# Kernel optimization log

Hardware: AMD Instinct MI355X
Metric: run time of the kernel (lower is better)

## Reference

```python
import math
import jax, jax.numpy as jnp
import numpy as np

S, K, Q, N, D, H = 512, 512, 64, 262144, 256, 8
DH = D // H
EPS = 1e-5


def layer_norm(x, g, b):
    mu = jnp.mean(x, axis=-1, keepdims=True)
    var = jnp.mean((x - mu) ** 2, axis=-1, keepdims=True)
    return (x - mu) / jnp.sqrt(var + EPS) * g + b


def setup_inputs() -> dict:
    key = jax.random.key(0)
    ks = jax.random.split(key, 12)
    s = 1.0 / math.sqrt(D)
    x = jax.random.normal(ks[0], (N, D), dtype=jnp.float32)
    target_ids = jax.random.randint(ks[1], (S, K), 0, N)
    # unique query slots per sample (matches torch per-slot overwrite with distinct ids)
    perm = jax.vmap(lambda k: jax.random.permutation(k, K))(jax.random.split(ks[2], S))
    add_ids = perm[:, :Q]
    return {
        "x": x,
        "target_ids": target_ids,
        "add_ids": add_ids,
        "Wq": jax.random.uniform(ks[3], (D, D), jnp.float32, -s, s),
        "bq": jnp.zeros((D,), jnp.float32),
        "Wk": jax.random.uniform(ks[4], (D, D), jnp.float32, -s, s),
        "bk": jnp.zeros((D,), jnp.float32),
        "Wv": jax.random.uniform(ks[5], (D, D), jnp.float32, -s, s),
        "bv": jnp.zeros((D,), jnp.float32),
        "g1": jnp.ones((D,), jnp.float32),
        "b1": jnp.zeros((D,), jnp.float32),
        "Wl": jax.random.uniform(ks[6], (D, D), jnp.float32, -s, s),
        "bl": jnp.zeros((D,), jnp.float32),
        "g2": jnp.ones((D,), jnp.float32),
        "b2": jnp.zeros((D,), jnp.float32),
    }


def reference(x, target_ids, add_ids, Wq, bq, Wk, bk, Wv, bv, g1, b1, Wl, bl, g2, b2):
    # gather per-sample node subsets
    key_t = x[target_ids]                                   # [S, K, D]
    query = jnp.take_along_axis(key_t, add_ids[:, :, None], axis=1)  # [S, Q, D]
    # MAB projections
    Qp = (query @ Wq.T + bq).reshape(S, Q, H, DH)
    Kp = (key_t @ Wk.T + bk).reshape(S, K, H, DH)
    Vp = (key_t @ Wv.T + bv).reshape(S, K, H, DH)
    # attention with original scaling by sqrt(dim_V) (full D, not per-head)
    scores = jnp.einsum("sqhd,skhd->shqk", Qp, Kp) / math.sqrt(D)
    A = jax.nn.softmax(scores, axis=-1)
    out = Qp + jnp.einsum("shqk,skhd->sqhd", A, Vp)          # residual on Q_
    out = out.reshape(S, Q, D)
    out = layer_norm(out, g1, b1)
    out = out + jax.nn.relu(out @ Wl.T + bl)
    out = layer_norm(out, g2, b2)                            # [S, Q, D]
    # scatter back into per-sample slots, then residual with key
    x_fuse = jnp.zeros((S, K, D), out.dtype)
    x_fuse = x_fuse.at[jnp.arange(S)[:, None], add_ids].set(out)
    x_fuse = x_fuse + key_t
    return x_fuse.reshape(S * K, D)
```

## Files before the change

### kernel.cpp

```cpp
#include <hip/hip_runtime.h>

#define S_ 512
#define K_ 512
#define Q_ 64
#define D_ 256
#define H_ 8
#define SK_ (S_*K_)
#define SQ_ (S_*Q_)

typedef float f32x4 __attribute__((ext_vector_type(4)));
typedef short bf16x8 __attribute__((ext_vector_type(8)));
typedef short bf16x4 __attribute__((ext_vector_type(4)));

__device__ __forceinline__ short f2bf(float f) {
  unsigned u = __builtin_bit_cast(unsigned, f);
  u += 0x7fffu + ((u >> 16) & 1u);
  return (short)(u >> 16);
}
__device__ __forceinline__ float bf2f(short s) {
  unsigned u = ((unsigned)(unsigned short)s) << 16;
  return __builtin_bit_cast(float, u);
}

__device__ __forceinline__ void async_copy16(short* lds, const short* g) {
  __builtin_amdgcn_global_load_lds(
      (const __attribute__((address_space(1))) void*)g,
      (__attribute__((address_space(3))) void*)lds, 16, 0, 0);
}

__global__ void cvt_w_kernel(const float* Wq, const float* Wk, const float* Wv,
                             const float* Wl, short* out) {
  int i = blockIdx.x * 256 + threadIdx.x;
  const float* src = (i < 65536) ? Wq : (i < 131072) ? Wk : (i < 196608) ? Wv : Wl;
  out[i] = f2bf(src[i & 65535]);
}

__global__ void expand_kernel(const short* kb, float* dout) {
  int g = blockIdx.x * 256 + threadIdx.x;
  bf16x8 v = *(const bf16x8*)(kb + (size_t)g * 8);
  f32x4 a, b;
#pragma unroll
  for (int j = 0; j < 4; j++) { a[j] = bf2f(v[j]); b[j] = bf2f(v[j + 4]); }
  *(f32x4*)(dout + (size_t)g * 8) = a;
  *(f32x4*)(dout + (size_t)g * 8 + 4) = b;
}

__global__ __launch_bounds__(256, 2) void gkv_kernel(const float* x, const int* tid,
                                                     const short* Wkb, const float* bkb,
                                                     const short* Wvb, const float* bvb,
                                                     short* kb, short* Kt, short* Vt) {
  __shared__ short As[128 * 256];
  int t = threadIdx.x;
  int w = t >> 6, lane = t & 63, quad = lane >> 4, l16 = lane & 15;
  int rbase0 = blockIdx.x * 128;
  int colbase = w * 64;

#pragma unroll
  for (int i = 0; i < 16; i++) {
    int g = i * 256 + t;
    int row = g >> 5, c = g & 31;
    int m = rbase0 + row;
    int src = tid[m];
    const float* xp = x + (size_t)src * 256 + c * 8;
    f32x4 v0 = *(const f32x4*)xp;
    f32x4 v1 = *(const f32x4*)(xp + 4);
    bf16x8 o;
#pragma unroll
    for (int j = 0; j < 4; j++) { o[j] = f2bf(v0[j]); o[j + 4] = f2bf(v1[j]); }
    *(bf16x8*)(kb + (size_t)m * 256 + c * 8) = o;
    *(bf16x8*)(As + row * 256 + (c ^ (row & 15)) * 8) = o;
  }
  __syncthreads();

#pragma unroll 1
  for (int p = 0; p < 2; p++) {
    const short* Wb = p ? Wvb : Wkb;
    const float* bias = p ? bvb : bkb;
    bf16x8 b[4][8];
#pragma unroll
    for (int nt = 0; nt < 4; nt++)
#pragma unroll
      for (int kk = 0; kk < 8; kk++)
        b[nt][kk] = *(const bf16x8*)(Wb + (colbase + nt * 16 + l16) * 256 + kk * 32 + quad * 8);
    float bv4[4];
#pragma unroll
    for (int nt = 0; nt < 4; nt++) bv4[nt] = bias[colbase + nt * 16 + l16];

    for (int mt = 0; mt < 8; mt++) {
      bf16x8 a[8];
#pragma unroll
      for (int kk = 0; kk < 8; kk++)
        a[kk] = *(const bf16x8*)(As + (mt * 16 + l16) * 256 + (((kk * 4 + quad) ^ l16) * 8));
      f32x4 acc[4];
#pragma unroll
      for (int nt = 0; nt < 4; nt++) acc[nt] = (f32x4){bv4[nt], bv4[nt], bv4[nt], bv4[nt]};
#pragma unroll
      for (int kk = 0; kk < 8; kk++)
#pragma unroll
        for (int nt = 0; nt < 4; nt++)
          acc[nt] = __builtin_amdgcn_mfma_f32_16x16x32_bf16(a[kk], b[nt][kk], acc[nt], 0, 0, 0);

      int rbase = rbase0 + mt * 16;
      int s = rbase >> 9;
      int keyb = (rbase & 511) + quad * 4;
      if (p == 0) {
#pragma unroll
        for (int nt = 0; nt < 4; nt++) {
          int col = colbase + nt * 16 + l16;
          int h = col >> 5, dh = col & 31;
          size_t basek = ((size_t)(s * 8 + h) * 512 + keyb) * 32 + dh;
#pragma unroll
          for (int r = 0; r < 4; r++) Kt[basek + (size_t)r * 32] = f2bf(acc[nt][r]);
        }
      } else {
#pragma unroll
        for (int nt = 0; nt < 4; nt++) {
          int col = colbase + nt * 16 + l16;
          int h = col >> 5, dh = col & 31;
          bf16x4 pk;
#pragma unroll
          for (int r = 0; r < 4; r++) pk[r] = f2bf(acc[nt][r]);
          *(bf16x4*)(Vt + ((((size_t)s * 8 + h) * 32 + dh) << 9) + keyb) = pk;
        }
      }
    }
  }
}

template<int INDEXED>
__global__ __launch_bounds__(256, 2) void gemm2_kernel(const short* A, const int* aid,
                                                       const short* Wb, const float* bias,
                                                       short* Cp) {
  __shared__ short As[128 * 256];
  int w = threadIdx.x >> 6, lane = threadIdx.x & 63;
  int quad = lane >> 4, l16 = lane & 15;
  int rbase0 = blockIdx.x * 128;
  int colbase = w * 64;

  bf16x8 b[4][8];
#pragma unroll
  for (int nt = 0; nt < 4; nt++)
#pragma unroll
    for (int kk = 0; kk < 8; kk++)
      b[nt][kk] = *(const bf16x8*)(Wb + (colbase + nt * 16 + l16) * 256 + kk * 32 + quad * 8);
  float bv[4];
#pragma unroll
  for (int nt = 0; nt < 4; nt++) bv[nt] = bias[colbase + nt * 16 + l16];

  int cc = lane & 31;
#pragma unroll
  for (int i = 0; i < 16; i++) {
    int chunkLinear = w * 1024 + i * 64 + lane;
    int row = chunkLinear >> 5;
    int c = cc ^ (row & 15);
    int m = rbase0 + row;
    int arow = INDEXED ? (((m >> 6) << 9) + aid[m]) : m;
    async_copy16(As + (size_t)(w * 1024 + i * 64) * 8,
                 A + (size_t)arow * 256 + c * 8);
  }
  __syncthreads();

  for (int mt = 0; mt < 8; mt++) {
    bf16x8 a[8];
#pragma unroll
    for (int kk = 0; kk < 8; kk++)
      a[kk] = *(const bf16x8*)(As + (mt * 16 + l16) * 256 + (((kk * 4 + quad) ^ l16) * 8));
    f32x4 acc[4];
#pragma unroll
    for (int nt = 0; nt < 4; nt++) acc[nt] = (f32x4){bv[nt], bv[nt], bv[nt], bv[nt]};
#pragma unroll
    for (int kk = 0; kk < 8; kk++)
#pragma unroll
      for (int nt = 0; nt < 4; nt++)
        acc[nt] = __builtin_amdgcn_mfma_f32_16x16x32_bf16(a[kk], b[nt][kk], acc[nt], 0, 0, 0);

    int rbase = rbase0 + mt * 16;
#pragma unroll
    for (int nt = 0; nt < 4; nt++) {
      int col = colbase + nt * 16 + l16;
#pragma unroll
      for (int r = 0; r < 4; r++)
        Cp[(size_t)(rbase + quad * 4 + r) * 256 + col] = f2bf(acc[nt][r]);
    }
  }
}

__global__ __launch_bounds__(256, 2) void attn_kernel(const short* Qp, const short* Kt,
                                                      const short* Vt, float* aout) {
  __shared__ short ldsK[16384];
  __shared__ short ldsV[16384];
  int bid = blockIdx.x;
  int s = bid >> 3, h = bid & 7;
  int w = threadIdx.x >> 6;
  int lane = threadIdx.x & 63;
  int quad = lane >> 4, l16 = lane & 15;

  const char* kb = (const char*)(Kt + ((size_t)bid << 14));
  const char* vb = (const char*)(Vt + ((size_t)bid << 14));
  char* lk = (char*)ldsK;
  char* lv = (char*)ldsV;

#pragma unroll
  for (int i = 0; i < 8; i++) {
    int ab = w * 8192 + i * 1024;
    int a = ab + lane * 16;
    async_copy16((short*)(lk + ab), (const short*)(kb + a));
    async_copy16((short*)(lv + ab), (const short*)(vb + (a ^ (((a >> 10) & 7) << 4))));
  }

  bf16x8 aq = *(const bf16x8*)(Qp + ((size_t)(s * 64 + w * 16 + l16)) * 256 + h * 32 + quad * 8);
  __syncthreads();

  f32x4 zero = (f32x4){0.f, 0.f, 0.f, 0.f};
  f32x4 sc[32];
#pragma unroll
  for (int nt = 0; nt < 32; nt++) {
    bf16x8 bk = *(const bf16x8*)(lk + (nt * 16 + l16) * 64 + quad * 16);
    sc[nt] = __builtin_amdgcn_mfma_f32_16x16x32_bf16(aq, bk, zero, 0, 0, 0);
  }

  float lsum[4];
#pragma unroll
  for (int r = 0; r < 4; r++) {
    float t[16];
#pragma unroll
    for (int i = 0; i < 16; i++) t[i] = fmaxf(sc[i][r], sc[i + 16][r]);
#pragma unroll
    for (int st = 8; st; st >>= 1)
#pragma unroll
      for (int i = 0; i < st; i++) t[i] = fmaxf(t[i], t[i + st]);
    float m = t[0];
#pragma unroll
    for (int off = 1; off < 16; off <<= 1) m = fmaxf(m, __shfl_xor(m, off, 64));
#pragma unroll
    for (int nt = 0; nt < 32; nt++) sc[nt][r] = __expf((sc[nt][r] - m) * 0.0625f);
    float u[16];
#pragma unroll
    for (int i = 0; i < 16; i++) u[i] = sc[i][r] + sc[i + 16][r];
#pragma unroll
    for (int st = 8; st; st >>= 1)
#pragma unroll
      for (int i = 0; i < st; i++) u[i] += u[i + st];
    float l = u[0];
#pragma unroll
    for (int off = 1; off < 16; off <<= 1) l += __shfl_xor(l, off, 64);
    lsum[r] = l;
  }

  __syncthreads();

  f32x4 o[2] = {zero, zero};
#pragma unroll
  for (int half = 0; half < 2; half++) {
#pragma unroll
    for (int nt = 0; nt < 16; nt++) {
      int ntg = half * 16 + nt;
#pragma unroll
      for (int r = 0; r < 4; r++) {
        int q = quad * 4 + r;
        *(short*)(lk + w * 8192 + q * 512 + ((nt * 32 + l16 * 2) ^ ((q & 7) << 4))) =
            f2bf(sc[ntg][r]);
      }
    }
#pragma unroll
    for (int kk = 0; kk < 8; kk++) {
      bf16x8 ap = *(const bf16x8*)(lk + w * 8192 + l16 * 512 +
                                   ((kk * 64 + quad * 16) ^ ((l16 & 7) << 4)));
#pragma unroll
      for (int nt2 = 0; nt2 < 2; nt2++) {
        int dh = nt2 * 16 + l16;
        const bf16x8* vp = (const bf16x8*)(lv + dh * 1024 +
            ((half * 512 + kk * 64 + quad * 16) ^ ((dh & 7) << 4)));
        o[nt2] = __builtin_amdgcn_mfma_f32_16x16x32_bf16(ap, *vp, o[nt2], 0, 0, 0);
      }
    }
  }

#pragma unroll
  for (int nt2 = 0; nt2 < 2; nt2++)
#pragma unroll
    for (int r = 0; r < 4; r++) {
      int q = w * 16 + quad * 4 + r;
      int dh = nt2 * 16 + l16;
      size_t oq = ((size_t)(s * 64 + q)) * 256 + h * 32 + dh;
      aout[oq] = bf2f(Qp[oq]) + o[nt2][r] / lsum[r];
    }
}

__global__ void ln1_kernel(const float* ain, const float* g1, const float* b1, short* out) {
  int g = blockIdx.x * 256 + threadIdx.x;
  int row = g >> 6, lane = g & 63;
  f32x4 v = *(const f32x4*)(ain + (size_t)row * 256 + lane * 4);
  float s = v[0] + v[1] + v[2] + v[3];
  float s2 = v[0]*v[0] + v[1]*v[1] + v[2]*v[2] + v[3]*v[3];
#pragma unroll
  for (int off = 1; off < 64; off <<= 1) { s += __shfl_xor(s, off, 64); s2 += __shfl_xor(s2, off, 64); }
  float mu = s * (1.f / 256.f);
  float var = s2 * (1.f / 256.f) - mu * mu;
  float inv = rsqrtf(var + 1e-5f);
  f32x4 gv = *(const f32x4*)(g1 + lane * 4);
  f32x4 bv = *(const f32x4*)(b1 + lane * 4);
  bf16x4 ov;
#pragma unroll
  for (int j = 0; j < 4; j++) ov[j] = f2bf((v[j] - mu) * inv * gv[j] + bv[j]);
  *(bf16x4*)(out + (size_t)row * 256 + lane * 4) = ov;
}

__global__ void ln2_kernel(const short* ln1, const short* tmp, const float* g2, const float* b2,
                           const int* aid, float* dout) {
  int g = blockIdx.x * 256 + threadIdx.x;
  int row = g >> 6, lane = g & 63;
  bf16x4 a = *(const bf16x4*)(ln1 + (size_t)row * 256 + lane * 4);
  bf16x4 t = *(const bf16x4*)(tmp + (size_t)row * 256 + lane * 4);
  float v[4];
#pragma unroll
  for (int j = 0; j < 4; j++) v[j] = bf2f(a[j]) + fmaxf(bf2f(t[j]), 0.f);
  float s = v[0] + v[1] + v[2] + v[3];
  float s2 = v[0]*v[0] + v[1]*v[1] + v[2]*v[2] + v[3]*v[3];
#pragma unroll
  for (int off = 1; off < 64; off <<= 1) { s += __shfl_xor(s, off, 64); s2 += __shfl_xor(s2, off, 64); }
  float mu = s * (1.f / 256.f);
  float var = s2 * (1.f / 256.f) - mu * mu;
  float inv = rsqrtf(var + 1e-5f);
  f32x4 gv = *(const f32x4*)(g2 + lane * 4);
  f32x4 bv = *(const f32x4*)(b2 + lane * 4);
  int sIdx = row >> 6;
  int tgt = aid[row];
  float* op = dout + ((size_t)(sIdx * 512 + tgt)) * 256 + lane * 4;
  f32x4 cur = *(f32x4*)op;
#pragma unroll
  for (int j = 0; j < 4; j++) cur[j] += (v[j] - mu) * inv * gv[j] + bv[j];
  *(f32x4*)op = cur;
}

extern "C" void kernel_launch(void* const* d_in, const int* in_sizes, int n_in,
                              void* d_out, int out_size, void* d_ws, size_t ws_size,
                              hipStream_t stream) {
  const float* x   = (const float*)d_in[0];
  const int* tid   = (const int*)d_in[1];
  const int* aid   = (const int*)d_in[2];
  const float* Wq  = (const float*)d_in[3];
  const float* bq  = (const float*)d_in[4];
  const float* Wk  = (const float*)d_in[5];
  const float* bk  = (const float*)d_in[6];
  const float* Wv  = (const float*)d_in[7];
  const float* bv  = (const float*)d_in[8];
  const float* g1  = (const float*)d_in[9];
  const float* b1  = (const float*)d_in[10];
  const float* Wl  = (const float*)d_in[11];
  const float* bl  = (const float*)d_in[12];
  const float* g2  = (const float*)d_in[13];
  const float* b2  = (const float*)d_in[14];
  float* out = (float*)d_out;

  char* base = (char*)d_ws;
  short* Wqb = (short*)base;
  short* Wkb = Wqb + 65536;
  short* Wvb = Wkb + 65536;
  short* Wlb = Wvb + 65536;
  size_t off = 4ull * 65536 * 2;
  short* kb   = (short*)(base + off); off += (size_t)SK_ * 256 * 2;
  short* Qpb  = (short*)(base + off); off += (size_t)SQ_ * 256 * 2;
  short* Kpb  = (short*)(base + off); off += (size_t)SK_ * 256 * 2;
  short* ln1b = Qpb;
  short* tmpb = Kpb;
  short* Vtb  = (short*)d_out;
  float* aout = (float*)((char*)d_out + (size_t)SK_ * 256 * 2);
  (void)ws_size; (void)in_sizes; (void)n_in; (void)out_size;

  cvt_w_kernel<<<1024, 256, 0, stream>>>(Wq, Wk, Wv, Wl, Wqb);
  gkv_kernel<<<SK_ / 128, 256, 0, stream>>>(x, tid, Wkb, bk, Wvb, bv, kb, Kpb, Vtb);
  gemm2_kernel<1><<<SQ_ / 128, 256, 0, stream>>>(kb, aid, Wqb, bq, Qpb);
  attn_kernel<<<S_ * H_, 256, 0, stream>>>(Qpb, Kpb, Vtb, aout);
  ln1_kernel<<<SQ_ / 4, 256, 0, stream>>>(aout, g1, b1, ln1b);
  gemm2_kernel<0><<<SQ_ / 128, 256, 0, stream>>>(ln1b, nullptr, Wlb, bl, tmpb);
  expand_kernel<<<SK_ / 8, 256, 0, stream>>>(kb, out);
  ln2_kernel<<<SQ_ / 4, 256, 0, stream>>>(ln1b, tmpb, g2, b2, aid, out);
}
```

Before: 784.3 us.

## Fuse key residual write into gather-KV kernel and drop bf16 key buffer

The gather+KV projection kernel now writes the gathered fp32 rows of x straight into the output with nontemporal stores. This removes the intermediate bf16 key buffer and the separate expand kernel that read it back. The Q projection gathers its rows directly from x via tid and aid instead of from that buffer. The gkv tile is halved to 64 rows with launch bounds raised to 4 blocks per CU, and all row loads are issued up front to increase memory-level parallelism. Vt and the attention output move from the output buffer into workspace, which raises workspace use, and Q-row gathers now hit fp32 x and so read twice the bytes.

```diff
diff --git a/kernel.cpp b/kernel.cpp
--- a/kernel.cpp
+++ b/kernel.cpp
@@ -35,39 +35,38 @@
   out[i] = f2bf(src[i & 65535]);
 }
 
-__global__ void expand_kernel(const short* kb, float* dout) {
-  int g = blockIdx.x * 256 + threadIdx.x;
-  bf16x8 v = *(const bf16x8*)(kb + (size_t)g * 8);
-  f32x4 a, b;
-#pragma unroll
-  for (int j = 0; j < 4; j++) { a[j] = bf2f(v[j]); b[j] = bf2f(v[j + 4]); }
-  *(f32x4*)(dout + (size_t)g * 8) = a;
-  *(f32x4*)(dout + (size_t)g * 8 + 4) = b;
-}
-
-__global__ __launch_bounds__(256, 2) void gkv_kernel(const float* x, const int* tid,
+__global__ __launch_bounds__(256, 4) void gkv_kernel(const float* x, const int* tid,
                                                      const short* Wkb, const float* bkb,
                                                      const short* Wvb, const float* bvb,
-                                                     short* kb, short* Kt, short* Vt) {
-  __shared__ short As[128 * 256];
+                                                     short* Kt, short* Vt, float* out) {
+  __shared__ short As[64 * 256];
   int t = threadIdx.x;
   int w = t >> 6, lane = t & 63, quad = lane >> 4, l16 = lane & 15;
-  int rbase0 = blockIdx.x * 128;
+  int rbase0 = blockIdx.x * 64;
   int colbase = w * 64;
 
-#pragma unroll
-  for (int i = 0; i < 16; i++) {
+  int src[8];
+#pragma unroll
+  for (int i = 0; i < 8; i++) src[i] = tid[rbase0 + ((i * 256 + t) >> 5)];
+  f32x4 xv[8][2];
+#pragma unroll
+  for (int i = 0; i < 8; i++) {
+    int c = (i * 256 + t) & 31;
+    const float* xp = x + (size_t)src[i] * 256 + c * 8;
+    xv[i][0] = *(const f32x4*)xp;
+    xv[i][1] = *(const f32x4*)(xp + 4);
+  }
+#pragma unroll
+  for (int i = 0; i < 8; i++) {
     int g = i * 256 + t;
     int row = g >> 5, c = g & 31;
     int m = rbase0 + row;
-    int src = tid[m];
-    const float* xp = x + (size_t)src * 256 + c * 8;
-    f32x4 v0 = *(const f32x4*)xp;
-    f32x4 v1 = *(const f32x4*)(xp + 4);
+    float* op = out + (size_t)m * 256 + c * 8;
+    __builtin_nontemporal_store(xv[i][0], (f32x4*)op);
+    __builtin_nontemporal_store(xv[i][1], (f32x4*)(op + 4));
     bf16x8 o;
 #pragma unroll
-    for (int j = 0; j < 4; j++) { o[j] = f2bf(v0[j]); o[j + 4] = f2bf(v1[j]); }
-    *(bf16x8*)(kb + (size_t)m * 256 + c * 8) = o;
+    for (int j = 0; j < 4; j++) { o[j] = f2bf(xv[i][0][j]); o[j + 4] = f2bf(xv[i][1][j]); }
     *(bf16x8*)(As + row * 256 + (c ^ (row & 15)) * 8) = o;
   }
   __syncthreads();
@@ -86,7 +85,7 @@
 #pragma unroll
     for (int nt = 0; nt < 4; nt++) bv4[nt] = bias[colbase + nt * 16 + l16];
 
-    for (int mt = 0; mt < 8; mt++) {
+    for (int mt = 0; mt < 4; mt++) {
       bf16x8 a[8];
 #pragma unroll
       for (int kk = 0; kk < 8; kk++)
@@ -128,11 +127,13 @@
 }
 
 template<int INDEXED>
-__global__ __launch_bounds__(256, 2) void gemm2_kernel(const short* A, const int* aid,
+__global__ __launch_bounds__(256, 2) void gemm2_kernel(const short* A, const float* x,
+                                                       const int* tid, const int* aid,
                                                        const short* Wb, const float* bias,
                                                        short* Cp) {
   __shared__ short As[128 * 256];
-  int w = threadIdx.x >> 6, lane = threadIdx.x & 63;
+  int t = threadIdx.x;
+  int w = t >> 6, lane = t & 63;
   int quad = lane >> 4, l16 = lane & 15;
   int rbase0 = blockIdx.x * 128;
   int colbase = w * 64;
@@ -147,16 +148,33 @@
 #pragma unroll
   for (int nt = 0; nt < 4; nt++) bv[nt] = bias[colbase + nt * 16 + l16];
 
-  int cc = lane & 31;
-#pragma unroll
-  for (int i = 0; i < 16; i++) {
-    int chunkLinear = w * 1024 + i * 64 + lane;
-    int row = chunkLinear >> 5;
-    int c = cc ^ (row & 15);
-    int m = rbase0 + row;
-    int arow = INDEXED ? (((m >> 6) << 9) + aid[m]) : m;
-    async_copy16(As + (size_t)(w * 1024 + i * 64) * 8,
-                 A + (size_t)arow * 256 + c * 8);
+  if (INDEXED) {
+#pragma unroll
+    for (int i = 0; i < 16; i++) {
+      int g = i * 256 + t;
+      int row = g >> 5, c = g & 31;
+      int m = rbase0 + row;
+      int s = m >> 6;
+      int srcr = tid[(s << 9) + aid[m]];
+      const float* xp = x + (size_t)srcr * 256 + c * 8;
+      f32x4 v0 = *(const f32x4*)xp;
+      f32x4 v1 = *(const f32x4*)(xp + 4);
+      bf16x8 o;
+#pragma unroll
+      for (int j = 0; j < 4; j++) { o[j] = f2bf(v0[j]); o[j + 4] = f2bf(v1[j]); }
+      *(bf16x8*)(As + row * 256 + (c ^ (row & 15)) * 8) = o;
+    }
+  } else {
+    int cc = lane & 31;
+#pragma unroll
+    for (int i = 0; i < 16; i++) {
+      int chunkLinear = w * 1024 + i * 64 + lane;
+      int row = chunkLinear >> 5;
+      int c = cc ^ (row & 15);
+      int m = rbase0 + row;
+      async_copy16(As + (size_t)(w * 1024 + i * 64) * 8,
+                   A + (size_t)m * 256 + c * 8);
+    }
   }
   __syncthreads();
 
@@ -359,21 +377,19 @@
   short* Wvb = Wkb + 65536;
   short* Wlb = Wvb + 65536;
   size_t off = 4ull * 65536 * 2;
-  short* kb   = (short*)(base + off); off += (size_t)SK_ * 256 * 2;
+  short* Ktb  = (short*)(base + off); off += (size_t)SK_ * 256 * 2;
+  short* Vtb  = (short*)(base + off); off += (size_t)SK_ * 256 * 2;
   short* Qpb  = (short*)(base + off); off += (size_t)SQ_ * 256 * 2;
-  short* Kpb  = (short*)(base + off); off += (size_t)SK_ * 256 * 2;
+  float* aout = (float*)(base + off); off += (size_t)SQ_ * 256 * 4;
   short* ln1b = Qpb;
-  short* tmpb = Kpb;
-  short* Vtb  = (short*)d_out;
-  float* aout = (float*)((char*)d_out + (size_t)SK_ * 256 * 2);
+  short* tmpb = Ktb;
   (void)ws_size; (void)in_sizes; (void)n_in; (void)out_size;
 
   cvt_w_kernel<<<1024, 256, 0, stream>>>(Wq, Wk, Wv, Wl, Wqb);
-  gkv_kernel<<<SK_ / 128, 256, 0, stream>>>(x, tid, Wkb, bk, Wvb, bv, kb, Kpb, Vtb);
-  gemm2_kernel<1><<<SQ_ / 128, 256, 0, stream>>>(kb, aid, Wqb, bq, Qpb);
-  attn_kernel<<<S_ * H_, 256, 0, stream>>>(Qpb, Kpb, Vtb, aout);
+  gkv_kernel<<<SK_ / 64, 256, 0, stream>>>(x, tid, Wkb, bk, Wvb, bv, Ktb, Vtb, out);
+  gemm2_kernel<1><<<SQ_ / 128, 256, 0, stream>>>(nullptr, x, tid, aid, Wqb, bq, Qpb);
+  attn_kernel<<<S_ * H_, 256, 0, stream>>>(Qpb, Ktb, Vtb, aout);
   ln1_kernel<<<SQ_ / 4, 256, 0, stream>>>(aout, g1, b1, ln1b);
-  gemm2_kernel<0><<<SQ_ / 128, 256, 0, stream>>>(ln1b, nullptr, Wlb, bl, tmpb);
-  expand_kernel<<<SK_ / 8, 256, 0, stream>>>(kb, out);
+  gemm2_kernel<0><<<SQ_ / 128, 256, 0, stream>>>(ln1b, nullptr, nullptr, nullptr, Wlb, bl, tmpb);
   ln2_kernel<<<SQ_ / 4, 256, 0, stream>>>(ln1b, tmpb, g2, b2, aid, out);
 }
```

After: 1.454 ms. 85.4% more time.
